# Optimization experiments

Hardware: AMD Instinct MI355X
Metric: run time of the kernel (lower is better)

## Reference

```python
import jax, jax.numpy as jnp
import numpy as np

FACTOR = -1.0  # RecurrentAdditiveCell(units=11, factor=-1)


def setup_inputs() -> dict:
    key = jax.random.key(0)
    B, S, F = 1024, 4096, 11
    x = jax.random.normal(key, (B, S, F), dtype=jnp.float32)
    initial_state = jnp.zeros((B, 1), dtype=jnp.float32)
    return {"x": x, "initial_state": initial_state}


def reference(x, initial_state):
    # Cell: state_t = state_{t-1} + FACTOR * x_t, unrolled over time.
    # Equivalent closed form: init (broadcast over feat) + FACTOR * cumsum(x, time).
    # return_sequences=True -> emit every step's state: [B, S, F]
    y = initial_state[:, None, :] + FACTOR * jnp.cumsum(x, axis=1)
    return y
```

## Files before the change

### kernel.cpp

```cpp
#include <hip/hip_runtime.h>


#define BATCH    1024
#define SEQ      4096
#define FEAT     11
#define FACTOR   (-1.0f)

#define NTHREADS 256
#define TS       512
#define NC       (SEQ / TS)
#define NBLK     (BATCH * NC)
#define TILE_F4  (TS * FEAT / 4)
#define VLMAX    6
#define NWAVE    (NTHREADS / 64)

template <int CTRL, int RM, int BM, bool BC>
__device__ __forceinline__ float dpp_src(float v) {
    int r = __builtin_amdgcn_update_dpp(0, __float_as_int(v), CTRL, RM, BM, BC);
    return __int_as_float(r);
}

__device__ __forceinline__ float wave_iscan(float x) {
    x += dpp_src<0x111, 0xf, 0xf, true >(x);
    x += dpp_src<0x112, 0xf, 0xf, true >(x);
    x += dpp_src<0x114, 0xf, 0xf, true >(x);
    x += dpp_src<0x118, 0xf, 0xf, true >(x);
    x += dpp_src<0x142, 0xa, 0xf, false>(x);
    x += dpp_src<0x143, 0xc, 0xf, false>(x);
    return x;
}

__device__ __forceinline__ void gload_lds16(const float4* g, float4* l) {
    __builtin_amdgcn_global_load_lds(
        (const __attribute__((address_space(1))) void*)g,
        (__attribute__((address_space(3))) void*)l, 16, 0, 0);
}

__global__ __launch_bounds__(NTHREADS, 8)
void partial_kernel(const float* __restrict__ x, float* __restrict__ partials) {
    __shared__ float4 tile[TILE_F4];
    __shared__ float  waveSum[NWAVE][FEAT];

    const int blk  = blockIdx.x;
    const int t    = threadIdx.x;
    const int lane = t & 63;
    const int wav  = t >> 6;
    const float4* xg = (const float4*)x + (size_t)blk * TILE_F4;

#pragma unroll
    for (int i = 0; i < VLMAX; ++i) {
        int idx = t + NTHREADS * i;
        if (idx < TILE_F4) gload_lds16(xg + idx, &tile[idx]);
    }
    __syncthreads();

    const float2* lds2 = (const float2*)tile;
    float s[FEAT];
#pragma unroll
    for (int f = 0; f < FEAT; ++f) s[f] = 0.0f;
#pragma unroll
    for (int m = 0; m < FEAT; ++m) {
        float2 q = lds2[FEAT * t + m];
        s[(2 * m) % FEAT]     += q.x;
        s[(2 * m + 1) % FEAT] += q.y;
    }
#pragma unroll
    for (int f = 0; f < FEAT; ++f) s[f] = wave_iscan(s[f]);
    if (lane == 63) {
#pragma unroll
        for (int f = 0; f < FEAT; ++f) waveSum[wav][f] = s[f];
    }
    __syncthreads();
    if (t < FEAT) {
        float p = waveSum[0][t] + waveSum[1][t] + waveSum[2][t] + waveSum[3][t];
        partials[(size_t)blk * FEAT + t] = p;
    }
}

__global__ __launch_bounds__(NTHREADS, 8)
void scan_kernel(const float* __restrict__ x,
                 const float* __restrict__ init_state,
                 const float* __restrict__ partials,
                 float* __restrict__ y) {
    __shared__ float4 tile[TILE_F4];
    __shared__ float  waveTot[NWAVE][FEAT];
    __shared__ float  offsh[FEAT];

    const int blk  = blockIdx.x;
    const int b    = blk >> 3;
    const int c    = blk & (NC - 1);
    const int t    = threadIdx.x;
    const int lane = t & 63;
    const int wav  = t >> 6;

    const float4* xg = (const float4*)x + (size_t)blk * TILE_F4;
    float4*       yg = (float4*)y + (size_t)blk * TILE_F4;
    const float init_v = init_state[b];

#pragma unroll
    for (int i = 0; i < VLMAX; ++i) {
        int idx = t + NTHREADS * i;
        if (idx < TILE_F4) gload_lds16(xg + idx, &tile[idx]);
    }
    if (t < FEAT) {
        float o = 0.0f;
#pragma unroll
        for (int cc = 0; cc < NC - 1; ++cc) {
            float pv = partials[(size_t)(b * NC + cc) * FEAT + t];
            if (cc < c) o += pv;
        }
        offsh[t] = o;
    }
    __syncthreads();

    const float2* lds2 = (const float2*)tile;
    float L[2 * FEAT];
#pragma unroll
    for (int m = 0; m < FEAT; ++m) {
        float2 q = lds2[FEAT * t + m];
        L[2 * m]     = q.x;
        L[2 * m + 1] = q.y;
    }
    float inc[FEAT];
#pragma unroll
    for (int f = 0; f < FEAT; ++f) {
        L[FEAT + f] += L[f];
        inc[f] = wave_iscan(L[FEAT + f]);
    }
    if (lane == 63) {
#pragma unroll
        for (int f = 0; f < FEAT; ++f) waveTot[wav][f] = inc[f];
    }
    __syncthreads();

    float2* ldsw = (float2*)tile;
#pragma unroll
    for (int f = 0; f < FEAT; ++f) {
        float off = offsh[f] + inc[f] - L[FEAT + f];
#pragma unroll
        for (int w = 0; w < NWAVE; ++w)
            if (w < wav) off += waveTot[w][f];
        L[f]        = init_v + FACTOR * (off + L[f]);
        L[FEAT + f] = init_v + FACTOR * (off + L[FEAT + f]);
    }
#pragma unroll
    for (int m = 0; m < FEAT; ++m)
        ldsw[FEAT * t + m] = make_float2(L[2 * m], L[2 * m + 1]);
    __syncthreads();

#pragma unroll
    for (int i = 0; i < VLMAX; ++i) {
        int idx = t + NTHREADS * i;
        if (idx < TILE_F4) yg[idx] = tile[idx];
    }
}

extern "C" void kernel_launch(void* const* d_in, const int* in_sizes, int n_in,
                              void* d_out, int out_size, void* d_ws, size_t ws_size,
                              hipStream_t stream) {
    const float* x    = (const float*)d_in[0];
    const float* init = (const float*)d_in[1];
    float*       y    = (float*)d_out;
    float*       part = (float*)d_ws;
    partial_kernel<<<dim3(NBLK), dim3(NTHREADS), 0, stream>>>(x, part);
    scan_kernel<<<dim3(NBLK), dim3(NTHREADS), 0, stream>>>(x, init, part, y);
}
```

Baseline: 346.1 us.

## Fuse two-pass scan into single-pass chained scan with ticket-ordered blocks

Replaces the separate partial-sum kernel and scan kernel with one kernel. Each block takes a dynamic ticket, publishes its chunk aggregate behind a release flag, then spin-waits on the flags of earlier chunks in the same batch row to build its offset. Input x is read once instead of twice, which should cut global memory traffic. In exchange it adds a memset, atomics, spin-waiting, and lower declared occupancy (launch bounds 6 instead of 8).

After: 854.1 us. +146.7%, slower.

```diff
diff --git a/kernel.cpp b/kernel.cpp
--- a/kernel.cpp
+++ b/kernel.cpp
@@ -13,6 +13,10 @@
 #define TILE_F4  (TS * FEAT / 4)
 #define VLMAX    6
 #define NWAVE    (NTHREADS / 64)
+
+#define WS_FLAGS_OFF  256
+#define WS_AGGS_OFF   33024
+#define WS_ZERO_BYTES 33024
 
 template <int CTRL, int RM, int BM, bool BC>
 __device__ __forceinline__ float dpp_src(float v) {
@@ -36,80 +40,36 @@
         (__attribute__((address_space(3))) void*)l, 16, 0, 0);
 }
 
-__global__ __launch_bounds__(NTHREADS, 8)
-void partial_kernel(const float* __restrict__ x, float* __restrict__ partials) {
-    __shared__ float4 tile[TILE_F4];
-    __shared__ float  waveSum[NWAVE][FEAT];
+__global__ __launch_bounds__(NTHREADS, 6)
+void chained_scan_kernel(const float* __restrict__ x,
+                         const float* __restrict__ init_state,
+                         float* __restrict__ y,
+                         unsigned* __restrict__ counter,
+                         unsigned* __restrict__ flags,
+                         float* __restrict__ aggs) {
+    __shared__ float4    tile[TILE_F4];
+    __shared__ float     waveTot[NWAVE][FEAT];
+    __shared__ float     offsh[FEAT];
+    __shared__ unsigned  ticket_sh;
 
-    const int blk  = blockIdx.x;
-    const int t    = threadIdx.x;
-    const int lane = t & 63;
-    const int wav  = t >> 6;
-    const float4* xg = (const float4*)x + (size_t)blk * TILE_F4;
-
-#pragma unroll
-    for (int i = 0; i < VLMAX; ++i) {
-        int idx = t + NTHREADS * i;
-        if (idx < TILE_F4) gload_lds16(xg + idx, &tile[idx]);
-    }
-    __syncthreads();
-
-    const float2* lds2 = (const float2*)tile;
-    float s[FEAT];
-#pragma unroll
-    for (int f = 0; f < FEAT; ++f) s[f] = 0.0f;
-#pragma unroll
-    for (int m = 0; m < FEAT; ++m) {
-        float2 q = lds2[FEAT * t + m];
-        s[(2 * m) % FEAT]     += q.x;
-        s[(2 * m + 1) % FEAT] += q.y;
-    }
-#pragma unroll
-    for (int f = 0; f < FEAT; ++f) s[f] = wave_iscan(s[f]);
-    if (lane == 63) {
-#pragma unroll
-        for (int f = 0; f < FEAT; ++f) waveSum[wav][f] = s[f];
-    }
-    __syncthreads();
-    if (t < FEAT) {
-        float p = waveSum[0][t] + waveSum[1][t] + waveSum[2][t] + waveSum[3][t];
-        partials[(size_t)blk * FEAT + t] = p;
-    }
-}
-
-__global__ __launch_bounds__(NTHREADS, 8)
-void scan_kernel(const float* __restrict__ x,
-                 const float* __restrict__ init_state,
-                 const float* __restrict__ partials,
-                 float* __restrict__ y) {
-    __shared__ float4 tile[TILE_F4];
-    __shared__ float  waveTot[NWAVE][FEAT];
-    __shared__ float  offsh[FEAT];
-
-    const int blk  = blockIdx.x;
-    const int b    = blk >> 3;
-    const int c    = blk & (NC - 1);
     const int t    = threadIdx.x;
     const int lane = t & 63;
     const int wav  = t >> 6;
 
-    const float4* xg = (const float4*)x + (size_t)blk * TILE_F4;
-    float4*       yg = (float4*)y + (size_t)blk * TILE_F4;
+    if (t == 0) ticket_sh = atomicAdd(counter, 1u);
+    __syncthreads();
+    const unsigned tk = ticket_sh;
+    const int b = (int)(tk >> 3);
+    const int c = (int)(tk & (NC - 1));
+
+    const float4* xg = (const float4*)x + (size_t)tk * TILE_F4;
+    float4*       yg = (float4*)y + (size_t)tk * TILE_F4;
     const float init_v = init_state[b];
 
 #pragma unroll
     for (int i = 0; i < VLMAX; ++i) {
         int idx = t + NTHREADS * i;
         if (idx < TILE_F4) gload_lds16(xg + idx, &tile[idx]);
-    }
-    if (t < FEAT) {
-        float o = 0.0f;
-#pragma unroll
-        for (int cc = 0; cc < NC - 1; ++cc) {
-            float pv = partials[(size_t)(b * NC + cc) * FEAT + t];
-            if (cc < c) o += pv;
-        }
-        offsh[t] = o;
     }
     __syncthreads();
 
@@ -130,6 +90,32 @@
     if (lane == 63) {
 #pragma unroll
         for (int f = 0; f < FEAT; ++f) waveTot[wav][f] = inc[f];
+    }
+    __syncthreads();
+
+    if (wav == 0 && lane < FEAT) {
+        float agg = waveTot[0][lane] + waveTot[1][lane]
+                  + waveTot[2][lane] + waveTot[3][lane];
+        __hip_atomic_store(&aggs[(size_t)tk * FEAT + lane], agg,
+                           __ATOMIC_RELAXED, __HIP_MEMORY_SCOPE_AGENT);
+    }
+    __syncthreads();
+    if (t == 0)
+        __hip_atomic_store(&flags[tk], 1u,
+                           __ATOMIC_RELEASE, __HIP_MEMORY_SCOPE_AGENT);
+
+    if (t < FEAT) {
+        float off = 0.0f;
+        for (int cc = 0; cc < c; ++cc) {
+            const unsigned pred = (unsigned)(b * NC + cc);
+            while (__hip_atomic_load(&flags[pred], __ATOMIC_ACQUIRE,
+                                     __HIP_MEMORY_SCOPE_AGENT) == 0u) {
+                __builtin_amdgcn_s_sleep(2);
+            }
+            off += __hip_atomic_load(&aggs[(size_t)pred * FEAT + t],
+                                     __ATOMIC_RELAXED, __HIP_MEMORY_SCOPE_AGENT);
+        }
+        offsh[t] = off;
     }
     __syncthreads();
 
@@ -161,7 +147,11 @@
     const float* x    = (const float*)d_in[0];
     const float* init = (const float*)d_in[1];
     float*       y    = (float*)d_out;
-    float*       part = (float*)d_ws;
-    partial_kernel<<<dim3(NBLK), dim3(NTHREADS), 0, stream>>>(x, part);
-    scan_kernel<<<dim3(NBLK), dim3(NTHREADS), 0, stream>>>(x, init, part, y);
+    unsigned*    cnt  = (unsigned*)d_ws;
+    unsigned*    flg  = (unsigned*)((char*)d_ws + WS_FLAGS_OFF);
+    float*       agg  = (float*)((char*)d_ws + WS_AGGS_OFF);
+
+    hipMemsetAsync(d_ws, 0, WS_ZERO_BYTES, stream);
+    chained_scan_kernel<<<dim3(NBLK), dim3(NTHREADS), 0, stream>>>(
+        x, init, y, cnt, flg, agg);
 }
```
